# Kernel tuning notes

Measured on AMD Instinct MI355X. Metric: run time of the kernel, lower is better.

## Reference

```python
import jax, jax.numpy as jnp
import numpy as np
from jax import lax

B, D, S, H, W, T = 128, 512, 30, 14, 14, 12


def setup_inputs() -> dict:
    key = jax.random.key(0)
    ks = jax.random.split(key, 28)
    f = lambda k, shape: jax.random.normal(k, shape, jnp.float32) * 0.05
    return {
        "q": f(ks[0], (B, D)),
        "cws": f(ks[1], (B, D, S)),
        "KB": f(ks[2], (B, D, H, W)),
        "c0": f(ks[3], (B, D)),
        "m0": f(ks[4], (B, D)),
        "Wq": f(ks[5], (D, D)), "bq": f(ks[6], (D,)),
        "Wct": f(ks[7], (2 * D, D)), "bct": f(ks[8], (D,)),
        "wca": f(ks[9], (D,)), "bca": f(ks[10], ()),
        "Wm": f(ks[11], (D, D)), "bm": f(ks[12], (D,)),
        "Wkb": f(ks[13], (D, D)), "bkb": f(ks[14], (D,)),
        "Wrm": f(ks[15], (2 * D, D)), "brm": f(ks[16], (D,)),
        "wra": f(ks[17], (D,)), "bra": f(ks[18], ()),
        "Wwm": f(ks[19], (2 * D, D)), "bwm": f(ks[20], (D,)),
        "wwa": f(ks[21], (D,)), "bwa": f(ks[22], ()),
        "Wam": f(ks[23], (2 * D, D)), "bam": f(ks[24], (D,)),
        "Wg": f(ks[25], (D, D)), "bg": f(ks[26], (D,)),
        "steps": T,
    }


def _mac(q, cws, KB, c0, m0, Wq, bq, Wct, bct, wca, bca, Wm, bm, Wkb, bkb,
         Wrm, brm, wra, bra, Wwm, bwm, wwa, bwa, Wam, bam, Wg, bg, steps):
    b, d, h, w = KB.shape[0], KB.shape[1], KB.shape[2], KB.shape[3]
    KBp = jnp.transpose(KB, (0, 2, 3, 1))          # B,H,W,d
    KB2 = KBp @ Wkb + bkb                           # KB_transform (step-invariant)
    q_i = q @ Wq + bq                               # q_transform (step-invariant)

    nhist = steps + 1
    c_hist = jnp.zeros((nhist, b, d), KB.dtype).at[0].set(c0)
    m_hist = jnp.zeros((nhist, b, d), KB.dtype).at[0].set(m0)

    def step(carry, t):
        c_hist, m_hist, c_prev, m_prev = carry
        # ---- ControlUnit ----
        cq = jnp.concatenate([q_i, c_prev], axis=-1) @ Wct + bct   # B,d
        clog = jnp.einsum('bds,d->bs', cq[:, :, None] * cws, wca) + bca
        cattn = jax.nn.softmax(clog, axis=-1)                       # B,S
        c_i = jnp.einsum('bs,bds->bd', cattn, cws)
        # ---- ReadUnit ----
        mp = m_prev @ Wm + bm                                       # B,d
        I = mp[:, None, None, :] * KB2                              # B,H,W,d
        Im = jnp.concatenate([I, KBp], axis=-1) @ Wrm + brm         # B,H,W,d
        rlog = jnp.einsum('bhwd,d->bhw', c_i[:, None, None, :] * Im, wra) + bra
        rattn = jax.nn.softmax(rlog.reshape(b, -1), axis=-1).reshape(b, h, w)
        m_new = jnp.einsum('bhw,bhwd->bd', rattn, KBp)
        # ---- WriteUnit (self_attn + mem_gate) ----
        _m = jnp.concatenate([m_new, m_prev], axis=-1) @ Wwm + bwm
        slog = jnp.einsum('tbd,d->bt', c_i[None] * c_hist, wwa) + bwa
        valid = jnp.arange(nhist) <= t
        slog = jnp.where(valid[None, :], slog, jnp.float32(-1e9))
        sattn = jax.nn.softmax(slog, axis=-1)                       # B,T+1
        m_sa = jnp.einsum('bt,tbd->bd', sattn, m_hist)
        _m = jnp.concatenate([m_sa, _m], axis=-1) @ Wam + bam
        g = jax.nn.sigmoid(c_i @ Wg + bg)
        _m = g * m_prev + (1.0 - g) * _m
        c_hist = c_hist.at[t + 1].set(c_i)
        m_hist = m_hist.at[t + 1].set(_m)
        return (c_hist, m_hist, c_i, _m), None

    (c_hist, m_hist, c_last, m_last), _ = lax.scan(
        step, (c_hist, m_hist, c0, m0), jnp.arange(steps))
    return m_last


def reference(q, cws, KB, c0, m0, Wq, bq, Wct, bct, wca, bca, Wm, bm, Wkb, bkb,
              Wrm, brm, wra, bra, Wwm, bwm, wwa, bwa, Wam, bam, Wg, bg, steps):
    return _mac(q, cws, KB, c0, m0, Wq, bq, Wct, bct, wca, bca, Wm, bm, Wkb, bkb,
                Wrm, brm, wra, bra, Wwm, bwm, wwa, bwa, Wam, bam, Wg, bg, steps)
```

## Files before the change

kernel.cpp:

```cpp
#include <hip/hip_runtime.h>
#include <cstdint>

#define BB 128
#define DD 512
#define SS 30
#define PP 196
#define TT 12
#define BD (BB*DD)

typedef unsigned short ushortT;
typedef unsigned int uintT;

__device__ __forceinline__ float bf2f(ushortT u)
{
    return __uint_as_float(((uintT)u) << 16);
}

struct GDesc {
    const float *A0, *A1;
    const float *W0, *W1;
    const float *bias;
    float *out;
    const float *e1;
    int nparts, epi, mblk, nblk, aux;
};
struct GPack { GDesc d[6]; };

__global__ __launch_bounds__(256)
void gemm4(GPack pk)
{
    GDesc d = pk.d[blockIdx.z];
    if ((int)blockIdx.x >= d.mblk || (int)blockIdx.y >= d.nblk) return;
    const int tid  = threadIdx.x;
    const int lane = tid & 63;
    const int wv   = __builtin_amdgcn_readfirstlane(tid >> 6);

    if (d.epi == 5) {
        int bb = (blockIdx.x * 4 + blockIdx.y) * 2;
        #pragma unroll
        for (int b = bb; b < bb + 2; ++b) {
            const float* sat = d.W0 + b * 16;
            float a0 = 0.f, a1 = 0.f;
            for (int tp = 0; tp <= d.aux; ++tp) {
                float s = sat[tp];
                const float* mh = d.A0 + (size_t)tp * BD + (size_t)b * DD;
                a0 = fmaf(s, mh[tid], a0);
                a1 = fmaf(s, mh[tid + 256], a1);
            }
            d.out[(size_t)b * DD + tid] = a0;
            d.out[(size_t)b * DD + tid + 256] = a1;
        }
        return;
    }

    const int m0 = blockIdx.x * 8;
    const int c0 = blockIdx.y * 128;
    float accx[8], accy[8];
    #pragma unroll
    for (int m = 0; m < 8; ++m) { accx[m] = 0.f; accy[m] = 0.f; }

    for (int p = 0; p < d.nparts; ++p) {
        const float* A = p ? d.A1 : d.A0;
        const float* W = p ? d.W1 : d.W0;
        const float* a = A + (size_t)m0 * 512 + wv * 128;
        const float2* Wb = (const float2*)(W + (size_t)(wv * 128) * 512 + c0) + lane;
        #pragma unroll 4
        for (int k = 0; k < 128; ++k) {
            float2 w2 = Wb[(size_t)k * 256];
            #pragma unroll
            for (int m = 0; m < 8; ++m) {
                float av = a[m * 512 + k];
                accx[m] = fmaf(av, w2.x, accx[m]);
                accy[m] = fmaf(av, w2.y, accy[m]);
            }
        }
    }

    __shared__ float red[4][8][128];
    #pragma unroll
    for (int m = 0; m < 8; ++m)
        *(float2*)&red[wv][m][lane * 2] = make_float2(accx[m], accy[m]);
    __syncthreads();

    for (int i = tid; i < 1024; i += 256) {
        int mm = i >> 7, cl = i & 127;
        float s = (red[0][mm][cl] + red[1][mm][cl])
                + (red[2][mm][cl] + red[3][mm][cl]);
        int row = m0 + mm, col = c0 + cl;
        size_t o = (size_t)row * 512 + col;
        if (d.epi == 0)      d.out[o] = s + d.bias[col];
        else if (d.epi == 1) { float v = s + d.bias[col];
                               d.out[o] = 1.f / (1.f + __expf(-v)); }
        else if (d.epi == 4) d.out[o] = s + d.e1[o];
        else                 d.out[o] = s;
    }
}

struct SP {
    const float *cq, *cws, *cwsT, *wca, *bca, *wra, *wwa, *bwa;
    float *c_hist, *sattn, *vb;
    const float *msa, *mnw, *gb, *b2, *Wam, *WA, *WB;
    float *m_hist, *dst;
    int t;
};

__global__ __launch_bounds__(512)
void stepA(SP P)
{
    const int tid = threadIdx.x;
    const int lane = tid & 63;
    __shared__ float cqw[512], ciw[512];
    __shared__ float clog2[32], cattn[32], slog[16];
    __shared__ float red[8][4][128];

    if ((int)blockIdx.x < 128) {
        if (P.t >= TT) return;
        int b = blockIdx.x, w = tid >> 6, t = P.t;
        cqw[tid] = P.cq[(size_t)b*DD + tid] * P.wca[tid];
        __syncthreads();
        for (int s = w; s < SS; s += 8) {
            const float* row = P.cwsT + ((size_t)b*SS + s)*DD;
            float a = 0.f;
            #pragma unroll
            for (int j = 0; j < 8; ++j)
                a = fmaf(cqw[lane + 64*j], row[lane + 64*j], a);
            for (int off = 32; off; off >>= 1) a += __shfl_xor(a, off, 64);
            if (lane == 0) clog2[s] = a;
        }
        __syncthreads();
        if (tid < 32) {
            float v = (tid < SS) ? clog2[tid] + P.bca[0] : -1e30f;
            float mx = v;
            for (int off = 16; off; off >>= 1) mx = fmaxf(mx, __shfl_xor(mx, off, 32));
            float e = (tid < SS) ? __expf(v - mx) : 0.f;
            float sm = e;
            for (int off = 16; off; off >>= 1) sm += __shfl_xor(sm, off, 32);
            cattn[tid] = e / sm;
        }
        __syncthreads();
        {
            const float* base = P.cws + (size_t)b*DD*SS + (size_t)tid*SS;
            float acc = 0.f;
            #pragma unroll
            for (int j = 0; j < SS; ++j) acc = fmaf(cattn[j], base[j], acc);
            P.c_hist[(size_t)(t+1)*BD + (size_t)b*DD + tid] = acc;
            P.vb[(size_t)b*DD + tid] = acc * P.wra[tid];
            ciw[tid] = acc * P.wwa[tid];
        }
        __syncthreads();
        for (int tp = tid >> 6; tp <= t; tp += 8) {
            const float* ch = P.c_hist + (size_t)tp*BD + (size_t)b*DD;
            float a = 0.f;
            #pragma unroll
            for (int j = 0; j < 8; ++j)
                a = fmaf(ciw[lane + 64*j], ch[lane + 64*j], a);
            for (int off = 32; off; off >>= 1) a += __shfl_xor(a, off, 64);
            if (lane == 0) slog[tp] = a;
        }
        __syncthreads();
        if (tid < 16) {
            float v = (tid <= t) ? slog[tid] + P.bwa[0] : -1e30f;
            float mx = v;
            for (int off = 8; off; off >>= 1) mx = fmaxf(mx, __shfl_xor(mx, off, 16));
            float e = (tid <= t) ? __expf(v - mx) : 0.f;
            float sm = e;
            for (int off = 8; off; off >>= 1) sm += __shfl_xor(sm, off, 16);
            P.sattn[b*16 + tid] = e / sm;
        }
    } else {
        if (P.t == 0) return;
        int gb_ = blockIdx.x - 128;
        int mt = gb_ >> 2, nc = gb_ & 3;
        int wv = __builtin_amdgcn_readfirstlane(tid >> 6);
        const int koff = wv * 64;
        const float* mprev = P.m_hist + (size_t)(P.t - 1) * BD;
        const int r0 = mt * 4;
        float ax[4] = {0.f,0.f,0.f,0.f}, ay[4] = {0.f,0.f,0.f,0.f};

        {
            const float* a = P.msa + (size_t)r0 * 512 + koff;
            const float2* Wb = (const float2*)(P.Wam + (size_t)koff * 512 + nc * 128) + lane;
            #pragma unroll 4
            for (int k = 0; k < 64; ++k) {
                float2 w2 = Wb[(size_t)k * 256];
                #pragma unroll
                for (int m = 0; m < 4; ++m) {
                    float av = a[m*512 + k];
                    ax[m] = fmaf(av, w2.x, ax[m]); ay[m] = fmaf(av, w2.y, ay[m]);
                }
            }
        }
        {
            const float* a = P.mnw + (size_t)r0 * 512 + koff;
            const float2* Wb = (const float2*)(P.WA + (size_t)koff * 512 + nc * 128) + lane;
            #pragma unroll 4
            for (int k = 0; k < 64; ++k) {
                float2 w2 = Wb[(size_t)k * 256];
                #pragma unroll
                for (int m = 0; m < 4; ++m) {
                    float av = a[m*512 + k];
                    ax[m] = fmaf(av, w2.x, ax[m]); ay[m] = fmaf(av, w2.y, ay[m]);
                }
            }
        }
        {
            const float* a = mprev + (size_t)r0 * 512 + koff;
            const float2* Wb = (const float2*)(P.WB + (size_t)koff * 512 + nc * 128) + lane;
            #pragma unroll 4
            for (int k = 0; k < 64; ++k) {
                float2 w2 = Wb[(size_t)k * 256];
                #pragma unroll
                for (int m = 0; m < 4; ++m) {
                    float av = a[m*512 + k];
                    ax[m] = fmaf(av, w2.x, ax[m]); ay[m] = fmaf(av, w2.y, ay[m]);
                }
            }
        }
        #pragma unroll
        for (int m = 0; m < 4; ++m)
            *(float2*)&red[wv][m][lane*2] = make_float2(ax[m], ay[m]);
        __syncthreads();
        {
            int mm = tid >> 7, cl = tid & 127;
            float s = 0.f;
            #pragma unroll
            for (int j = 0; j < 8; ++j) s += red[j][mm][cl];
            int row = r0 + mm, col = nc*128 + cl;
            size_t o = (size_t)row*512 + col;
            float v = s + P.b2[col];
            float g = P.gb[o];
            float pv = mprev[o];
            P.dst[o] = g*pv + (1.f - g)*v;
        }
    }
}

__global__ __launch_bounds__(256)
void read1y(const ushortT* __restrict__ KBh, const float* __restrict__ ubuf,
            const float* __restrict__ mp, const float* __restrict__ WkbT,
            const float* __restrict__ vW, float* __restrict__ rlogp)
{
    int b = blockIdx.x, dg = blockIdx.y, tid = threadIdx.x;
    int lane = tid & 63, w = tid >> 6;
    __shared__ float red[4][64];
    __shared__ float yb[64];
    {
        const float* ur = ubuf + (size_t)b*512;
        const float* mr = mp + (size_t)b*512;
        const float* Wc = WkbT + dg*64 + lane;
        float s = 0.f;
        for (int k = w*128; k < w*128 + 128; ++k)
            s = fmaf(ur[k]*mr[k], Wc[(size_t)k*512], s);
        red[w][lane] = s;
    }
    __syncthreads();
    if (tid < 64)
        yb[tid] = (red[0][tid]+red[1][tid]) + (red[2][tid]+red[3][tid])
                + vW[(size_t)b*512 + dg*64 + tid];
    __syncthreads();
    float a0=0.f, a1=0.f, a2=0.f, a3=0.f;
    if (tid < PP) {
        const ushortT* kb = KBh + ((size_t)b*512 + dg*64)*PP + tid;
        #pragma unroll 4
        for (int dd = 0; dd < 64; dd += 4) {
            a0 = fmaf(bf2f(kb[(size_t)(dd+0)*PP]), yb[dd+0], a0);
            a1 = fmaf(bf2f(kb[(size_t)(dd+1)*PP]), yb[dd+1], a1);
            a2 = fmaf(bf2f(kb[(size_t)(dd+2)*PP]), yb[dd+2], a2);
            a3 = fmaf(bf2f(kb[(size_t)(dd+3)*PP]), yb[dd+3], a3);
        }
    }
    rlogp[((size_t)b*8 + dg)*256 + tid] = (a0+a1)+(a2+a3);
}

__global__ __launch_bounds__(256)
void read2(const ushortT* __restrict__ KBh, const float* __restrict__ rlogp,
           float* __restrict__ m_new)
{
    int b = blockIdx.x, dg = blockIdx.y;
    int tid = threadIdx.x, lane = tid & 63, w = tid >> 6;
    __shared__ float ex[256];
    __shared__ float wred[4];

    float v = -1e30f;
    if (tid < PP) {
        const float* rp = rlogp + (size_t)b*2048 + tid;
        float t0 = rp[0]    + rp[256];
        float t1 = rp[512]  + rp[768];
        float t2 = rp[1024] + rp[1280];
        float t3 = rp[1536] + rp[1792];
        v = (t0+t1)+(t2+t3);
    }
    float mx = v;
    for (int off = 32; off; off >>= 1) mx = fmaxf(mx, __shfl_xor(mx, off, 64));
    if (lane == 0) wred[w] = mx;
    __syncthreads();
    float gmax = fmaxf(fmaxf(wred[0], wred[1]), fmaxf(wred[2], wred[3]));
    float e = (tid < PP) ? __expf(v - gmax) : 0.f;
    float sm = e;
    for (int off = 32; off; off >>= 1) sm += __shfl_xor(sm, off, 64);
    __syncthreads();
    if (lane == 0) wred[w] = sm;
    __syncthreads();
    float inv = 1.f / ((wred[0]+wred[1]) + (wred[2]+wred[3]));
    ex[tid] = e * inv;
    __syncthreads();

    #pragma unroll 2
    for (int i = 0; i < 16; ++i) {
        int d = dg*64 + w*16 + i;
        const ushortT* row = KBh + ((size_t)b*512 + d)*PP;
        float a = ex[lane]       * bf2f(row[lane])
                + ex[lane + 64]  * bf2f(row[lane + 64])
                + ex[lane + 128] * bf2f(row[lane + 128]);
        if (lane < PP - 192) a = fmaf(ex[lane + 192], bf2f(row[lane + 192]), a);
        for (int off = 32; off; off >>= 1) a += __shfl_xor(a, off, 64);
        if (lane == 0) m_new[(size_t)b*512 + d] = a;
    }
}

struct SetupP {
    const float *Wrm, *Wkb, *cws, *KB, *c0v, *m0v, *bwm, *Wam_bot, *bam;
    float *WrmTu, *WrmTv, *WkbT, *cwsT, *c_hist, *m_hist, *b2;
    ushortT *KBh;
};

__global__ __launch_bounds__(256)
void setup_misc(SetupP P)
{
    __shared__ float tile[32][33];
    int id = blockIdx.x, tid = threadIdx.x;

    if (id < 768) {
        int which = id >> 8, tj = id & 255;
        const float* src = (which == 0) ? P.Wrm
                         : (which == 1) ? (P.Wrm + 512*512) : P.Wkb;
        float* dst = (which == 0) ? P.WrmTu : (which == 1) ? P.WrmTv : P.WkbT;
        int bx = (tj & 15) * 32, by = (tj >> 4) * 32;
        int tx = tid & 31, ty = tid >> 5;
        #pragma unroll
        for (int i = 0; i < 32; i += 8)
            tile[ty+i][tx] = src[(size_t)(by+ty+i)*512 + bx+tx];
        __syncthreads();
        #pragma unroll
        for (int i = 0; i < 32; i += 8)
            dst[(size_t)(bx+ty+i)*512 + by+tx] = tile[tx][ty+i];
    } else if (id < 2816) {
        int j = id - 768;
        int b = j >> 4, dc = j & 15;
        const float* src = P.cws + ((size_t)b*DD + dc*32) * SS;
        for (int i = tid; i < 1024; i += 256) {
            int r = i >> 5, s = i & 31;
            if (s < SS) tile[r][s] = src[(size_t)r*SS + s];
        }
        __syncthreads();
        for (int i = tid; i < 1024; i += 256) {
            int s = i >> 5, r = i & 31;
            if (s < SS)
                P.cwsT[((size_t)b*SS + s)*DD + dc*32 + r] = tile[r][s];
        }
    } else if (id < 9088) {
        size_t i = ((size_t)(id - 2816) * 256 + tid) * 8;
        #pragma unroll
        for (int j = 0; j < 8; ++j) {
            uintT bits = __float_as_uint(P.KB[i + j]);
            uintT r = (bits + 0x7FFFu + ((bits >> 16) & 1u)) >> 16;
            P.KBh[i + j] = (ushortT)r;
        }
    } else if (id < 9344) {
        int i = (id - 9088) * 256 + tid;
        P.c_hist[i] = P.c0v[i];
        P.m_hist[i] = P.m0v[i];
    } else {
        int lane = tid & 63, w = tid >> 6;
        int n = (id - 9344) * 64 + lane;
        float s = 0.f;
        for (int k = w*128; k < w*128 + 128; ++k)
            s = fmaf(P.bwm[k], P.Wam_bot[(size_t)k*512 + n], s);
        __shared__ float red[4][64];
        red[w][lane] = s;
        __syncthreads();
        if (tid < 64) {
            int nn = (id - 9344) * 64 + tid;
            P.b2[nn] = red[0][tid] + red[1][tid] + red[2][tid] + red[3][tid]
                     + P.bam[nn];
        }
    }
}

extern "C" void kernel_launch(void* const* d_in, const int* in_sizes, int n_in,
                              void* d_out, int out_size, void* d_ws, size_t ws_size,
                              hipStream_t stream)
{
    (void)in_sizes; (void)n_in; (void)out_size; (void)ws_size;
    const float* q   = (const float*)d_in[0];
    const float* cws = (const float*)d_in[1];
    const float* KB  = (const float*)d_in[2];
    const float* c0  = (const float*)d_in[3];
    const float* m0  = (const float*)d_in[4];
    const float* Wq  = (const float*)d_in[5];
    const float* bq  = (const float*)d_in[6];
    const float* Wct = (const float*)d_in[7];
    const float* bct = (const float*)d_in[8];
    const float* wca = (const float*)d_in[9];
    const float* bca = (const float*)d_in[10];
    const float* Wm  = (const float*)d_in[11];
    const float* bm  = (const float*)d_in[12];
    const float* Wkb = (const float*)d_in[13];
    const float* Wrm = (const float*)d_in[15];
    const float* wra = (const float*)d_in[17];
    const float* Wwm = (const float*)d_in[19];
    const float* bwm = (const float*)d_in[20];
    const float* wwa = (const float*)d_in[21];
    const float* bwa = (const float*)d_in[22];
    const float* Wam = (const float*)d_in[23];
    const float* bam = (const float*)d_in[24];
    const float* Wg  = (const float*)d_in[25];
    const float* bg  = (const float*)d_in[26];

    float* ws      = (float*)d_ws;
    float* c_hist  = ws;
    float* m_hist  = ws + 13*BD;
    float* qct     = ws + 26*BD;
    float* q_i     = ws + 27*BD;
    float* cq      = ws + 28*BD;
    float* mp      = ws + 29*BD;
    float* vb      = ws + 30*BD;
    float* ubuf    = ws + 31*BD;
    float* vW      = ws + 32*BD;
    float* gb      = ws + 33*BD;
    float* msa     = ws + 34*BD;
    float* mnw     = ws + 35*BD;
    float* sattn   = ws + 36*BD;
    float* rlogp   = ws + 37*BD;
    float* WrmTu   = ws + 41*BD;
    float* WrmTv   = ws + 45*BD;
    float* WkbT   = ws + 49*BD;
    float* WA      = ws + 53*BD;
    float* WB      = ws + 57*BD;
    float* b2      = ws + 61*BD;
    float* cwsT    = ws + 62*BD;
    ushortT* KBh   = (ushortT*)(ws + 92*BD);

    const float* Wct_bot = Wct + 512*512;
    const float* Wam_bot = Wam + 512*512;
    const float* Wwm_bot = Wwm + 512*512;
    dim3 blk(256);
    GDesc Z = { nullptr,nullptr,nullptr,nullptr,nullptr,nullptr,nullptr,
                1, 6, 0, 0, 0 };

    {
        SetupP S;
        S.Wrm = Wrm; S.Wkb = Wkb; S.cws = cws; S.KB = KB;
        S.c0v = c0; S.m0v = m0; S.bwm = bwm; S.Wam_bot = Wam_bot; S.bam = bam;
        S.WrmTu = WrmTu; S.WrmTv = WrmTv; S.WkbT = WkbT; S.cwsT = cwsT;
        S.c_hist = c_hist; S.m_hist = m_hist; S.b2 = b2; S.KBh = KBh;
        setup_misc<<<dim3(9352), blk, 0, stream>>>(S);
    }
    {
        GPack pk;
        pk.d[0] = { Wwm, nullptr, Wam_bot, nullptr, nullptr, WA, nullptr,
                    1, 6, 64, 4, 0 };
        pk.d[1] = { Wwm_bot, nullptr, Wam_bot, nullptr, nullptr, WB, nullptr,
                    1, 6, 64, 4, 0 };
        pk.d[2] = { q, nullptr, Wq, nullptr, bq, q_i, nullptr,
                    1, 0, 16, 4, 0 };
        pk.d[3] = Z; pk.d[4] = Z; pk.d[5] = Z;
        gemm4<<<dim3(64,4,3), blk, 0, stream>>>(pk);
    }
    {
        GPack pk;
        pk.d[0] = { q_i, nullptr, Wct, nullptr, bct, qct, nullptr,
                    1, 0, 16, 4, 0 };
        pk.d[1] = { q_i, c0, Wct, Wct_bot, bct, cq, nullptr,
                    2, 0, 16, 4, 0 };
        pk.d[2] = Z; pk.d[3] = Z; pk.d[4] = Z; pk.d[5] = Z;
        gemm4<<<dim3(16,4,2), blk, 0, stream>>>(pk);
    }

    for (int t = 0; t <= TT; ++t) {
        {
            SP P;
            P.cq = cq; P.cws = cws; P.cwsT = cwsT;
            P.wca = wca; P.bca = bca; P.wra = wra; P.wwa = wwa; P.bwa = bwa;
            P.c_hist = c_hist; P.sattn = sattn; P.vb = vb;
            P.msa = msa; P.mnw = mnw; P.gb = gb; P.b2 = b2;
            P.Wam = Wam; P.WA = WA; P.WB = WB;
            P.m_hist = m_hist;
            P.dst = (t == TT) ? (float*)d_out : (m_hist + (size_t)t * BD);
            P.t = t;
            stepA<<<dim3(256), dim3(512), 0, stream>>>(P);
        }
        if (t == TT) break;

        float* c_i = c_hist + (size_t)(t+1) * BD;
        {
            GPack pk;
            pk.d[0] = { vb, nullptr, WrmTu, nullptr, nullptr, ubuf, nullptr,
                        1, 6, 16, 4, 0 };
            pk.d[1] = { vb, nullptr, WrmTv, nullptr, nullptr, vW, nullptr,
                        1, 6, 16, 4, 0 };
            pk.d[2] = { c_i, nullptr, Wg, nullptr, bg, gb, nullptr,
                        1, 1, 16, 4, 0 };
            pk.d[3] = { c_i, nullptr, Wct_bot, nullptr, nullptr, cq, qct,
                        1, 4, 16, 4, 0 };
            pk.d[4] = { m_hist + (size_t)t * BD, nullptr, Wm, nullptr, bm, mp,
                        nullptr, 1, 0, 16, 4, 0 };
            pk.d[5] = { m_hist, nullptr, sattn, nullptr, nullptr, msa, nullptr,
                        1, 5, 16, 4, t };
            gemm4<<<dim3(16,4,6), blk, 0, stream>>>(pk);
        }
        read1y<<<dim3(BB,8), blk, 0, stream>>>(KBh, ubuf, mp, WkbT, vW, rlogp);
        read2<<<dim3(BB,8), blk, 0, stream>>>(KBh, rlogp, mnw);
    }
}
```

Measured before the change: 833.6 us.

## Shrink GEMM tiles for more blocks and store step weights in bf16

Per-block GEMM tiles shrink from 8x128 to 2x256 outputs using float4 weight loads, and the tail GEMM in stepA moves from 4 to 2 rows per block with 384 blocks. The grid grows from 64 to 128 blocks per GEMM so more CUs work on the small batched matmuls. The precomputed WA, WB and Wam weights and the transposed cws are stored as bf16 to halve the bytes read every step. In exchange, weights are reread more often per output row, and bf16 rounding lowers precision.

```diff
diff --git a/kernel.cpp b/kernel.cpp
--- a/kernel.cpp
+++ b/kernel.cpp
@@ -14,6 +14,11 @@
 __device__ __forceinline__ float bf2f(ushortT u)
 {
     return __uint_as_float(((uintT)u) << 16);
+}
+__device__ __forceinline__ ushortT f2bf(float f)
+{
+    uintT b = __float_as_uint(f);
+    return (ushortT)((b + 0x7FFFu + ((b >> 16) & 1u)) >> 16);
 }
 
 struct GDesc {
@@ -36,54 +41,48 @@
     const int wv   = __builtin_amdgcn_readfirstlane(tid >> 6);
 
     if (d.epi == 5) {
-        int bb = (blockIdx.x * 4 + blockIdx.y) * 2;
-        #pragma unroll
-        for (int b = bb; b < bb + 2; ++b) {
-            const float* sat = d.W0 + b * 16;
-            float a0 = 0.f, a1 = 0.f;
-            for (int tp = 0; tp <= d.aux; ++tp) {
-                float s = sat[tp];
-                const float* mh = d.A0 + (size_t)tp * BD + (size_t)b * DD;
-                a0 = fmaf(s, mh[tid], a0);
-                a1 = fmaf(s, mh[tid + 256], a1);
-            }
-            d.out[(size_t)b * DD + tid] = a0;
-            d.out[(size_t)b * DD + tid + 256] = a1;
-        }
+        int b = blockIdx.x * 2 + blockIdx.y;
+        const float* sat = d.W0 + b * 16;
+        float a0 = 0.f, a1 = 0.f;
+        for (int tp = 0; tp <= d.aux; ++tp) {
+            float s = sat[tp];
+            const float* mh = d.A0 + (size_t)tp * BD + (size_t)b * DD;
+            a0 = fmaf(s, mh[tid], a0);
+            a1 = fmaf(s, mh[tid + 256], a1);
+        }
+        d.out[(size_t)b * DD + tid] = a0;
+        d.out[(size_t)b * DD + tid + 256] = a1;
         return;
     }
 
-    const int m0 = blockIdx.x * 8;
-    const int c0 = blockIdx.y * 128;
-    float accx[8], accy[8];
-    #pragma unroll
-    for (int m = 0; m < 8; ++m) { accx[m] = 0.f; accy[m] = 0.f; }
+    const int m0 = blockIdx.x * 2;
+    const int c0 = blockIdx.y * 256;
+    float acc0x = 0.f, acc0y = 0.f, acc0z = 0.f, acc0w = 0.f;
+    float acc1x = 0.f, acc1y = 0.f, acc1z = 0.f, acc1w = 0.f;
 
     for (int p = 0; p < d.nparts; ++p) {
         const float* A = p ? d.A1 : d.A0;
         const float* W = p ? d.W1 : d.W0;
         const float* a = A + (size_t)m0 * 512 + wv * 128;
-        const float2* Wb = (const float2*)(W + (size_t)(wv * 128) * 512 + c0) + lane;
+        const float4* Wb = (const float4*)(W + (size_t)(wv * 128) * 512 + c0) + lane;
         #pragma unroll 4
         for (int k = 0; k < 128; ++k) {
-            float2 w2 = Wb[(size_t)k * 256];
-            #pragma unroll
-            for (int m = 0; m < 8; ++m) {
-                float av = a[m * 512 + k];
-                accx[m] = fmaf(av, w2.x, accx[m]);
-                accy[m] = fmaf(av, w2.y, accy[m]);
-            }
-        }
-    }
-
-    __shared__ float red[4][8][128];
-    #pragma unroll
-    for (int m = 0; m < 8; ++m)
-        *(float2*)&red[wv][m][lane * 2] = make_float2(accx[m], accy[m]);
-    __syncthreads();
-
-    for (int i = tid; i < 1024; i += 256) {
-        int mm = i >> 7, cl = i & 127;
+            float4 w4 = Wb[(size_t)k * 128];
+            float a0 = a[k], a1 = a[512 + k];
+            acc0x = fmaf(a0, w4.x, acc0x);  acc1x = fmaf(a1, w4.x, acc1x);
+            acc0y = fmaf(a0, w4.y, acc0y);  acc1y = fmaf(a1, w4.y, acc1y);
+            acc0z = fmaf(a0, w4.z, acc0z);  acc1z = fmaf(a1, w4.z, acc1z);
+            acc0w = fmaf(a0, w4.w, acc0w);  acc1w = fmaf(a1, w4.w, acc1w);
+        }
+    }
+
+    __shared__ float red[4][2][256];
+    *(float4*)&red[wv][0][lane * 4] = make_float4(acc0x, acc0y, acc0z, acc0w);
+    *(float4*)&red[wv][1][lane * 4] = make_float4(acc1x, acc1y, acc1z, acc1w);
+    __syncthreads();
+
+    for (int i = tid; i < 512; i += 256) {
+        int mm = i >> 8, cl = i & 255;
         float s = (red[0][mm][cl] + red[1][mm][cl])
                 + (red[2][mm][cl] + red[3][mm][cl]);
         int row = m0 + mm, col = c0 + cl;
@@ -92,14 +91,17 @@
         else if (d.epi == 1) { float v = s + d.bias[col];
                                d.out[o] = 1.f / (1.f + __expf(-v)); }
         else if (d.epi == 4) d.out[o] = s + d.e1[o];
+        else if (d.epi == 7) ((ushortT*)d.out)[o] = f2bf(s);
         else                 d.out[o] = s;
     }
 }
 
 struct SP {
-    const float *cq, *cws, *cwsT, *wca, *bca, *wra, *wwa, *bwa;
+    const float *cq, *cws, *wca, *bca, *wra, *wwa, *bwa;
+    const ushortT *cwsTh;
     float *c_hist, *sattn, *vb;
-    const float *msa, *mnw, *gb, *b2, *Wam, *WA, *WB;
+    const float *msa, *mnw, *gb, *b2;
+    const ushortT *WamH, *WAH, *WBH;
     float *m_hist, *dst;
     int t;
 };
@@ -111,7 +113,7 @@
     const int lane = tid & 63;
     __shared__ float cqw[512], ciw[512];
     __shared__ float clog2[32], cattn[32], slog[16];
-    __shared__ float red[8][4][128];
+    __shared__ float red[8][2][128];
 
     if ((int)blockIdx.x < 128) {
         if (P.t >= TT) return;
@@ -119,11 +121,11 @@
         cqw[tid] = P.cq[(size_t)b*DD + tid] * P.wca[tid];
         __syncthreads();
         for (int s = w; s < SS; s += 8) {
-            const float* row = P.cwsT + ((size_t)b*SS + s)*DD;
+            const ushortT* row = P.cwsTh + ((size_t)b*SS + s)*DD;
             float a = 0.f;
             #pragma unroll
             for (int j = 0; j < 8; ++j)
-                a = fmaf(cqw[lane + 64*j], row[lane + 64*j], a);
+                a = fmaf(cqw[lane + 64*j], bf2f(row[lane + 64*j]), a);
             for (int off = 32; off; off >>= 1) a += __shfl_xor(a, off, 64);
             if (lane == 0) clog2[s] = a;
         }
@@ -174,53 +176,29 @@
         int wv = __builtin_amdgcn_readfirstlane(tid >> 6);
         const int koff = wv * 64;
         const float* mprev = P.m_hist + (size_t)(P.t - 1) * BD;
-        const int r0 = mt * 4;
-        float ax[4] = {0.f,0.f,0.f,0.f}, ay[4] = {0.f,0.f,0.f,0.f};
-
-        {
-            const float* a = P.msa + (size_t)r0 * 512 + koff;
-            const float2* Wb = (const float2*)(P.Wam + (size_t)koff * 512 + nc * 128) + lane;
-            #pragma unroll 4
+        const int r0 = mt * 2;
+        float ax0 = 0.f, ay0 = 0.f, ax1 = 0.f, ay1 = 0.f;
+
+        const float* As[3] = { P.msa, P.mnw, mprev };
+        const ushortT* Ws[3] = { P.WamH, P.WAH, P.WBH };
+        #pragma unroll
+        for (int seg = 0; seg < 3; ++seg) {
+            const float* a = As[seg] + (size_t)r0 * 512 + koff;
+            const uintT* Wb = (const uintT*)(Ws[seg] + (size_t)koff * 512 + nc * 128) + lane;
+            #pragma unroll 8
             for (int k = 0; k < 64; ++k) {
-                float2 w2 = Wb[(size_t)k * 256];
-                #pragma unroll
-                for (int m = 0; m < 4; ++m) {
-                    float av = a[m*512 + k];
-                    ax[m] = fmaf(av, w2.x, ax[m]); ay[m] = fmaf(av, w2.y, ay[m]);
-                }
+                uintT w = Wb[(size_t)k * 256];
+                float wx = __uint_as_float(w << 16);
+                float wy = __uint_as_float(w & 0xFFFF0000u);
+                float av0 = a[k], av1 = a[512 + k];
+                ax0 = fmaf(av0, wx, ax0); ay0 = fmaf(av0, wy, ay0);
+                ax1 = fmaf(av1, wx, ax1); ay1 = fmaf(av1, wy, ay1);
             }
         }
-        {
-            const float* a = P.mnw + (size_t)r0 * 512 + koff;
-            const float2* Wb = (const float2*)(P.WA + (size_t)koff * 512 + nc * 128) + lane;
-            #pragma unroll 4
-            for (int k = 0; k < 64; ++k) {
-                float2 w2 = Wb[(size_t)k * 256];
-                #pragma unroll
-                for (int m = 0; m < 4; ++m) {
-                    float av = a[m*512 + k];
-                    ax[m] = fmaf(av, w2.x, ax[m]); ay[m] = fmaf(av, w2.y, ay[m]);
-                }
-            }
-        }
-        {
-            const float* a = mprev + (size_t)r0 * 512 + koff;
-            const float2* Wb = (const float2*)(P.WB + (size_t)koff * 512 + nc * 128) + lane;
-            #pragma unroll 4
-            for (int k = 0; k < 64; ++k) {
-                float2 w2 = Wb[(size_t)k * 256];
-                #pragma unroll
-                for (int m = 0; m < 4; ++m) {
-                    float av = a[m*512 + k];
-                    ax[m] = fmaf(av, w2.x, ax[m]); ay[m] = fmaf(av, w2.y, ay[m]);
-                }
-            }
-        }
-        #pragma unroll
-        for (int m = 0; m < 4; ++m)
-            *(float2*)&red[wv][m][lane*2] = make_float2(ax[m], ay[m]);
-        __syncthreads();
-        {
+        *(float2*)&red[wv][0][lane*2] = make_float2(ax0, ay0);
+        *(float2*)&red[wv][1][lane*2] = make_float2(ax1, ay1);
+        __syncthreads();
+        if (tid < 256) {
             int mm = tid >> 7, cl = tid & 127;
             float s = 0.f;
             #pragma unroll
@@ -319,9 +297,9 @@
 }
 
 struct SetupP {
-    const float *Wrm, *Wkb, *cws, *KB, *c0v, *m0v, *bwm, *Wam_bot, *bam;
-    float *WrmTu, *WrmTv, *WkbT, *cwsT, *c_hist, *m_hist, *b2;
-    ushortT *KBh;
+    const float *Wrm, *Wkb, *cws, *KB, *c0v, *m0v, *bwm, *Wam, *Wam_bot, *bam;
+    float *WrmTu, *WrmTv, *WkbT, *c_hist, *m_hist, *b2;
+    ushortT *KBh, *cwsTh, *WamH;
 };
 
 __global__ __launch_bounds__(256)
@@ -356,7 +334,7 @@
         for (int i = tid; i < 1024; i += 256) {
             int s = i >> 5, r = i & 31;
             if (s < SS)
-                P.cwsT[((size_t)b*SS + s)*DD + dc*32 + r] = tile[r][s];
+                P.cwsTh[((size_t)b*SS + s)*DD + dc*32 + r] = f2bf(tile[r][s]);
         }
     } else if (id < 9088) {
         size_t i = ((size_t)(id - 2816) * 256 + tid) * 8;
@@ -370,7 +348,7 @@
         int i = (id - 9088) * 256 + tid;
         P.c_hist[i] = P.c0v[i];
         P.m_hist[i] = P.m0v[i];
-    } else {
+    } else if (id < 9352) {
         int lane = tid & 63, w = tid >> 6;
         int n = (id - 9344) * 64 + lane;
         float s = 0.f;
@@ -384,6 +362,11 @@
             P.b2[nn] = red[0][tid] + red[1][tid] + red[2][tid] + red[3][tid]
                      + P.bam[nn];
         }
+    } else {
+        size_t i = ((size_t)(id - 9352) * 256 + tid) * 8;
+        #pragma unroll
+        for (int j = 0; j < 8; ++j)
+            P.WamH[i + j] = f2bf(P.Wam[i + j]);
     }
 }
 
@@ -434,12 +417,13 @@
     float* rlogp   = ws + 37*BD;
     float* WrmTu   = ws + 41*BD;
     float* WrmTv   = ws + 45*BD;
-    float* WkbT   = ws + 49*BD;
-    float* WA      = ws + 53*BD;
-    float* WB      = ws + 57*BD;
+    float* WkbT    = ws + 49*BD;
     float* b2      = ws + 61*BD;
-    float* cwsT    = ws + 62*BD;
+    ushortT* cwsTh = (ushortT*)(ws + 62*BD);
     ushortT* KBh   = (ushortT*)(ws + 92*BD);
+    ushortT* WamH  = (ushortT*)(ws + 190*BD);
+    ushortT* WAH   = (ushortT*)(ws + 192*BD);
+    ushortT* WBH   = (ushortT*)(ws + 194*BD);
 
     const float* Wct_bot = Wct + 512*512;
     const float* Wam_bot = Wam + 512*512;
@@ -451,44 +435,46 @@
     {
         SetupP S;
         S.Wrm = Wrm; S.Wkb = Wkb; S.cws = cws; S.KB = KB;
-        S.c0v = c0; S.m0v = m0; S.bwm = bwm; S.Wam_bot = Wam_bot; S.bam = bam;
-        S.WrmTu = WrmTu; S.WrmTv = WrmTv; S.WkbT = WkbT; S.cwsT = cwsT;
-        S.c_hist = c_hist; S.m_hist = m_hist; S.b2 = b2; S.KBh = KBh;
-        setup_misc<<<dim3(9352), blk, 0, stream>>>(S);
+        S.c0v = c0; S.m0v = m0; S.bwm = bwm; S.Wam = Wam;
+        S.Wam_bot = Wam_bot; S.bam = bam;
+        S.WrmTu = WrmTu; S.WrmTv = WrmTv; S.WkbT = WkbT;
+        S.c_hist = c_hist; S.m_hist = m_hist; S.b2 = b2;
+        S.KBh = KBh; S.cwsTh = cwsTh; S.WamH = WamH;
+        setup_misc<<<dim3(9480), blk, 0, stream>>>(S);
     }
     {
         GPack pk;
-        pk.d[0] = { Wwm, nullptr, Wam_bot, nullptr, nullptr, WA, nullptr,
-                    1, 6, 64, 4, 0 };
-        pk.d[1] = { Wwm_bot, nullptr, Wam_bot, nullptr, nullptr, WB, nullptr,
-                    1, 6, 64, 4, 0 };
+        pk.d[0] = { Wwm, nullptr, Wam_bot, nullptr, nullptr, (float*)WAH,
+                    nullptr, 1, 7, 256, 2, 0 };
+        pk.d[1] = { Wwm_bot, nullptr, Wam_bot, nullptr, nullptr, (float*)WBH,
+                    nullptr, 1, 7, 256, 2, 0 };
         pk.d[2] = { q, nullptr, Wq, nullptr, bq, q_i, nullptr,
-                    1, 0, 16, 4, 0 };
+                    1, 0, 64, 2, 0 };
         pk.d[3] = Z; pk.d[4] = Z; pk.d[5] = Z;
-        gemm4<<<dim3(64,4,3), blk, 0, stream>>>(pk);
+        gemm4<<<dim3(256,2,3), blk, 0, stream>>>(pk);
     }
     {
         GPack pk;
         pk.d[0] = { q_i, nullptr, Wct, nullptr, bct, qct, nullptr,
-                    1, 0, 16, 4, 0 };
+                    1, 0, 64, 2, 0 };
         pk.d[1] = { q_i, c0, Wct, Wct_bot, bct, cq, nullptr,
-                    2, 0, 16, 4, 0 };
+                    2, 0, 64, 2, 0 };
         pk.d[2] = Z; pk.d[3] = Z; pk.d[4] = Z; pk.d[5] = Z;
-        gemm4<<<dim3(16,4,2), blk, 0, stream>>>(pk);
+        gemm4<<<dim3(64,2,2), blk, 0, stream>>>(pk);
     }
 
     for (int t = 0; t <= TT; ++t) {
         {
             SP P;
-            P.cq = cq; P.cws = cws; P.cwsT = cwsT;
+            P.cq = cq; P.cws = cws; P.cwsTh = cwsTh;
             P.wca = wca; P.bca = bca; P.wra = wra; P.wwa = wwa; P.bwa = bwa;
             P.c_hist = c_hist; P.sattn = sattn; P.vb = vb;
             P.msa = msa; P.mnw = mnw; P.gb = gb; P.b2 = b2;
-            P.Wam = Wam; P.WA = WA; P.WB = WB;
+            P.WamH = WamH; P.WAH = WAH; P.WBH = WBH;
             P.m_hist = m_hist;
             P.dst = (t == TT) ? (float*)d_out : (m_hist + (size_t)t * BD);
             P.t = t;
-            stepA<<<dim3(256), dim3(512), 0, stream>>>(P);
+            stepA<<<dim3(384), dim3(512), 0, stream>>>(P);
         }
         if (t == TT) break;
 
@@ -496,18 +482,18 @@
         {
             GPack pk;
             pk.d[0] = { vb, nullptr, WrmTu, nullptr, nullptr, ubuf, nullptr,
-                        1, 6, 16, 4, 0 };
+                        1, 6, 64, 2, 0 };
             pk.d[1] = { vb, nullptr, WrmTv, nullptr, nullptr, vW, nullptr,
-                        1, 6, 16, 4, 0 };
+                        1, 6, 64, 2, 0 };
             pk.d[2] = { c_i, nullptr, Wg, nullptr, bg, gb, nullptr,
-                        1, 1, 16, 4, 0 };
+                        1, 1, 64, 2, 0 };
             pk.d[3] = { c_i, nullptr, Wct_bot, nullptr, nullptr, cq, qct,
-                        1, 4, 16, 4, 0 };
+                        1, 4, 64, 2, 0 };
             pk.d[4] = { m_hist + (size_t)t * BD, nullptr, Wm, nullptr, bm, mp,
-                        nullptr, 1, 0, 16, 4, 0 };
+                        nullptr, 1, 0, 64, 2, 0 };
             pk.d[5] = { m_hist, nullptr, sattn, nullptr, nullptr, msa, nullptr,
-                        1, 5, 16, 4, t };
-            gemm4<<<dim3(16,4,6), blk, 0, stream>>>(pk);
+                        1, 5, 64, 2, t };
+            gemm4<<<dim3(64,2,6), blk, 0, stream>>>(pk);
         }
         read1y<<<dim3(BB,8), blk, 0, stream>>>(KBh, ubuf, mp, WkbT, vW, rlogp);
         read2<<<dim3(BB,8), blk, 0, stream>>>(KBh, rlogp, mnw);
```

Measured after the change: 776.4 us. -6.9%, faster.
